# Kernel tuning notes

Hardware: AMD Instinct MI355X
Metric: run time of the kernel (lower is better)

Reference implementation:

```python
import jax, jax.numpy as jnp
import numpy as np

B, N, D = 8, 1024, 768      # batch, n_patches, prototype dim
V, C, Hh = 30000, 512, 768  # vocab size, clip_text_dim, proj hidden dim
TEMPERATURE = 0.2
BN_EPS = 1e-5


def _l2norm(x, axis=-1, eps=1e-12):
    # matches torch F.normalize (clamp_min on the norm)
    n = jnp.linalg.norm(x, axis=axis, keepdims=True)
    return x / jnp.maximum(n, eps)


def setup_inputs() -> dict:
    key = jax.random.key(0)
    k = jax.random.split(key, 6)
    patch_tokens = jax.random.normal(k[0], (B, N, D), dtype=jnp.float32)
    vocab_clip_embeddings = jax.random.normal(k[1], (V, C), dtype=jnp.float32)
    # ProjectionHead params: Linear(C->Hh, no bias) + BN(Hh) + ReLU + Linear(Hh->D, bias)
    W1 = jax.random.normal(k[2], (C, Hh), dtype=jnp.float32) / np.sqrt(C)
    bn_gamma = jnp.ones((Hh,), dtype=jnp.float32)
    bn_beta = jnp.zeros((Hh,), dtype=jnp.float32)
    W2 = jax.random.normal(k[3], (Hh, D), dtype=jnp.float32) / np.sqrt(Hh)
    b2 = jnp.zeros((D,), dtype=jnp.float32)
    return {
        "patch_tokens": patch_tokens,
        "vocab_clip_embeddings": vocab_clip_embeddings,
        "W1": W1,
        "bn_gamma": bn_gamma,
        "bn_beta": bn_beta,
        "W2": W2,
        "b2": b2,
    }


def reference(patch_tokens, vocab_clip_embeddings, W1, bn_gamma, bn_beta, W2, b2):
    # vocab CLIP embeddings are L2-normalized at module init
    vocab = _l2norm(vocab_clip_embeddings)            # [V, C]
    # ProjectionHead (training-mode BatchNorm over the V "batch" dim)
    h = vocab @ W1                                    # [V, Hh]
    mean = jnp.mean(h, axis=0)
    var = jnp.var(h, axis=0)                          # biased, as torch BN uses
    h = (h - mean) * (bn_gamma / jnp.sqrt(var + BN_EPS)) + bn_beta
    h = jax.nn.relu(h)
    prototypes = _l2norm(h @ W2 + b2)                 # [V, D]
    # normalize patch tokens, compute patch-prototype logits
    pt = _l2norm(patch_tokens)                        # [B, N, D]
    patch_prototype_logits = jnp.einsum("bnd,vd->bnv", pt, prototypes)  # [B, N, V]
    vocab_logits = jnp.max(patch_prototype_logits, axis=1)              # [B, V]
    mixture_weights = jax.nn.softmax(vocab_logits / TEMPERATURE, axis=-1)
    return mixture_weights
```

## Files before the change

kernel.cpp:

```cpp
#include <hip/hip_runtime.h>
#include <hip/hip_bf16.h>
#include <cstdint>


#define CDIV(a,b) (((a)+(b)-1)/(b))

using bf16x8 = __attribute__((ext_vector_type(8))) __bf16;
using f32x4  = __attribute__((ext_vector_type(4))) float;
using u16x8  = __attribute__((ext_vector_type(8))) unsigned short;
using u16x4  = __attribute__((ext_vector_type(4))) unsigned short;
using u32x4  = __attribute__((ext_vector_type(4))) unsigned;

__device__ __forceinline__ unsigned short f2bf(float x) {
  unsigned u = __float_as_uint(x);
  u += 0x7fffu + ((u >> 16) & 1u);
  return (unsigned short)(u >> 16);
}
__device__ __forceinline__ float bf2f(unsigned short b) {
  return __uint_as_float(((unsigned)b) << 16);
}
__device__ __forceinline__ unsigned fkey(float x) {
  unsigned u = __float_as_uint(x);
  return (u & 0x80000000u) ? ~u : (u | 0x80000000u);
}
__device__ __forceinline__ float fdec(unsigned k) {
  unsigned u = (k & 0x80000000u) ? (k ^ 0x80000000u) : ~k;
  return __uint_as_float(u);
}

__global__ __launch_bounds__(512, 1)
void gemm256_max_kernel(const unsigned short* __restrict__ A,
                        const unsigned short* __restrict__ B,
                        unsigned* __restrict__ maxkey)
{
  constexpr int K = 768, NT = 12, NXT = 118;
  __shared__ __align__(16) unsigned short lds[8 * 8192];

  const int tid = threadIdx.x;
  const int w = tid >> 6, lane = tid & 63;
  const int lr = lane & 15, kg = lane >> 4;
  const int wr = w >> 2, wc = w & 3;

  const int bid = blockIdx.x;
  const int wg = (bid & 7) * 472 + (bid >> 3);
  const long m0 = (long)(wg / NXT) * 256;
  const long n0 = (long)(wg % NXT) * 256;

  auto stage = [&](int slot, int tk, int mat, int h) {
    const unsigned short* src = mat ? B : A;
    const long row0 = mat ? n0 : m0;
    unsigned short* dst = lds + (((slot * 2) + mat) * 2 + h) * 8192;
#pragma unroll
    for (int ld = 0; ld < 2; ++ld) {
      const int lc  = ld * 512 + tid;
      const int row = lc >> 2;
      const int qc  = (lc & 3) ^ ((row >> 1) & 3);
      const unsigned short* gp = src + (row0 + row) * K + tk * 64 + h * 32 + qc * 8;
      __builtin_amdgcn_global_load_lds(
          (const __attribute__((address_space(1))) void*)gp,
          (__attribute__((address_space(3))) void*)(dst + (ld * 512 + (w << 6)) * 8),
          16, 0, 0);
    }
  };
  auto rdA = [&](int s, int h, int fm) -> bf16x8 {
    const int row = wr * 128 + fm * 16 + lr;
    const int pc  = kg ^ ((row >> 1) & 3);
    return *(const bf16x8*)(lds + ((s * 2 + 0) * 2 + h) * 8192 + row * 32 + pc * 8);
  };
  auto rdB = [&](int s, int h, int fn) -> bf16x8 {
    const int row = wc * 64 + fn * 16 + lr;
    const int pc  = kg ^ ((row >> 1) & 3);
    return *(const bf16x8*)(lds + ((s * 2 + 1) * 2 + h) * 8192 + row * 32 + pc * 8);
  };

  f32x4 acc[8][4];
#pragma unroll
  for (int i = 0; i < 8; ++i)
#pragma unroll
    for (int j = 0; j < 4; ++j) acc[i][j] = f32x4{0.f, 0.f, 0.f, 0.f};

  stage(0, 0, 0, 0); stage(0, 0, 1, 0); stage(0, 0, 0, 1);
  stage(0, 0, 1, 1); stage(1, 1, 0, 0); stage(1, 1, 1, 0);
  asm volatile("s_waitcnt vmcnt(8)" ::: "memory");
  __builtin_amdgcn_s_barrier();

  bf16x8 a[4], b[4];
  auto tile_body = [&](int t, int s) {
    const int t1c = (t + 1 < NT) ? t + 1 : NT - 1;
    const int t2c = (t + 2 < NT) ? t + 2 : NT - 1;
    const int s1  = s ^ 1;

#pragma unroll
    for (int i = 0; i < 4; ++i) a[i] = rdA(s, 0, i);
#pragma unroll
    for (int i = 0; i < 4; ++i) b[i] = rdB(s, 0, i);
    stage(s1, t1c, 0, 1);
    __builtin_amdgcn_s_barrier();
    asm volatile("s_waitcnt lgkmcnt(0)" ::: "memory");
    __builtin_amdgcn_sched_barrier(0);
    __builtin_amdgcn_s_setprio(1);
#pragma unroll
    for (int fm = 0; fm < 4; ++fm)
#pragma unroll
      for (int fn = 0; fn < 4; ++fn)
        acc[fm][fn] = __builtin_amdgcn_mfma_f32_16x16x32_bf16(a[fm], b[fn], acc[fm][fn], 0, 0, 0);
    __builtin_amdgcn_s_setprio(0);
    __builtin_amdgcn_sched_barrier(0);
    __builtin_amdgcn_s_barrier();

#pragma unroll
    for (int i = 0; i < 4; ++i) a[i] = rdA(s, 0, 4 + i);
    stage(s1, t1c, 1, 1);
    __builtin_amdgcn_s_barrier();
    asm volatile("s_waitcnt lgkmcnt(0)" ::: "memory");
    __builtin_amdgcn_sched_barrier(0);
    __builtin_amdgcn_s_setprio(1);
#pragma unroll
    for (int fm = 0; fm < 4; ++fm)
#pragma unroll
      for (int fn = 0; fn < 4; ++fn)
        acc[4 + fm][fn] = __builtin_amdgcn_mfma_f32_16x16x32_bf16(a[fm], b[fn], acc[4 + fm][fn], 0, 0, 0);
    __builtin_amdgcn_s_setprio(0);
    asm volatile("s_waitcnt vmcnt(8)" ::: "memory");
    __builtin_amdgcn_sched_barrier(0);
    __builtin_amdgcn_s_barrier();

#pragma unroll
    for (int i = 0; i < 4; ++i) a[i] = rdA(s, 1, i);
#pragma unroll
    for (int i = 0; i < 4; ++i) b[i] = rdB(s, 1, i);
    stage(s, t2c, 0, 0);
    __builtin_amdgcn_s_barrier();
    asm volatile("s_waitcnt lgkmcnt(0)" ::: "memory");
    __builtin_amdgcn_sched_barrier(0);
    __builtin_amdgcn_s_setprio(1);
#pragma unroll
    for (int fm = 0; fm < 4; ++fm)
#pragma unroll
      for (int fn = 0; fn < 4; ++fn)
        acc[fm][fn] = __builtin_amdgcn_mfma_f32_16x16x32_bf16(a[fm], b[fn], acc[fm][fn], 0, 0, 0);
    __builtin_amdgcn_s_setprio(0);
    __builtin_amdgcn_sched_barrier(0);
    __builtin_amdgcn_s_barrier();

#pragma unroll
    for (int i = 0; i < 4; ++i) a[i] = rdA(s, 1, 4 + i);
    stage(s, t2c, 1, 0);
    __builtin_amdgcn_s_barrier();
    asm volatile("s_waitcnt lgkmcnt(0)" ::: "memory");
    __builtin_amdgcn_sched_barrier(0);
    __builtin_amdgcn_s_setprio(1);
#pragma unroll
    for (int fm = 0; fm < 4; ++fm)
#pragma unroll
      for (int fn = 0; fn < 4; ++fn)
        acc[4 + fm][fn] = __builtin_amdgcn_mfma_f32_16x16x32_bf16(a[fm], b[fn], acc[4 + fm][fn], 0, 0, 0);
    __builtin_amdgcn_s_setprio(0);
    asm volatile("s_waitcnt vmcnt(8)" ::: "memory");
    __builtin_amdgcn_sched_barrier(0);
    __builtin_amdgcn_s_barrier();
  };

  for (int tt = 0; tt < NT; tt += 2) { tile_body(tt, 0); tile_body(tt + 1, 1); }

  const int bb = (int)(m0 >> 10);
#pragma unroll
  for (int fn = 0; fn < 4; ++fn) {
    float mx = acc[0][fn][0];
#pragma unroll
    for (int fm = 0; fm < 8; ++fm)
#pragma unroll
      for (int j = 0; j < 4; ++j) mx = fmaxf(mx, acc[fm][fn][j]);
    mx = fmaxf(mx, __shfl_xor(mx, 16));
    mx = fmaxf(mx, __shfl_xor(mx, 32));
    const long gn = n0 + wc * 64 + fn * 16 + lr;
    if (lane < 16)
      atomicMax(maxkey + (long)bb * 30208 + gn, fkey(mx));
  }
}

template<int EPI, bool STATS>
__global__ __launch_bounds__(256)
void gemm_nt_kernel(const unsigned short* __restrict__ A,
                    const unsigned short* __restrict__ B,
                    unsigned short* __restrict__ Cout,
                    const float* __restrict__ bias,
                    float* __restrict__ sums,
                    int M, int N, int K)
{
  __shared__ __align__(16) unsigned short As[128 * 32];
  __shared__ __align__(16) unsigned short Bs[128 * 32];
  const int tid  = threadIdx.x;
  const int w    = tid >> 6, lane = tid & 63;
  const int m0   = blockIdx.y * 128, n0 = blockIdx.x * 128;
  const int wr   = w >> 1, wc = w & 1;
  const int lrow = lane & 15, kg = lane >> 4;

  f32x4 acc[4][4];
#pragma unroll
  for (int i = 0; i < 4; ++i)
#pragma unroll
    for (int j = 0; j < 4; ++j) acc[i][j] = f32x4{0.f, 0.f, 0.f, 0.f};

  for (int k0 = 0; k0 < K; k0 += 32) {
#pragma unroll
    for (int i = 0; i < 2; ++i) {
      const int li = w * 2 + i;
      const int c  = li * 64 + lane;
      const int r  = c >> 2;
      const int kc = (c & 3) * 8;
      {
        int row = m0 + r; if (row > M - 1) row = M - 1;
        const unsigned short* gp = A + (size_t)row * K + (k0 + kc);
        __builtin_amdgcn_global_load_lds(
            (const __attribute__((address_space(1))) void*)gp,
            (__attribute__((address_space(3))) void*)(As + li * 512), 16, 0, 0);
      }
      {
        int row = n0 + r; if (row > N - 1) row = N - 1;
        const unsigned short* gp = B + (size_t)row * K + (k0 + kc);
        __builtin_amdgcn_global_load_lds(
            (const __attribute__((address_space(1))) void*)gp,
            (__attribute__((address_space(3))) void*)(Bs + li * 512), 16, 0, 0);
      }
    }
    __syncthreads();

    bf16x8 af[4], bfr[4];
#pragma unroll
    for (int fm = 0; fm < 4; ++fm)
      af[fm] = *(const bf16x8*)(As + (wr * 64 + fm * 16 + lrow) * 32 + kg * 8);
#pragma unroll
    for (int fn = 0; fn < 4; ++fn)
      bfr[fn] = *(const bf16x8*)(Bs + (wc * 64 + fn * 16 + lrow) * 32 + kg * 8);

#pragma unroll
    for (int fm = 0; fm < 4; ++fm)
#pragma unroll
      for (int fn = 0; fn < 4; ++fn)
        acc[fm][fn] = __builtin_amdgcn_mfma_f32_16x16x32_bf16(
            af[fm], bfr[fn], acc[fm][fn], 0, 0, 0);
    __syncthreads();
  }

#pragma unroll
  for (int fm = 0; fm < 4; ++fm) {
    const int gmb = m0 + wr * 64 + fm * 16 + kg * 4;
#pragma unroll
    for (int fn = 0; fn < 4; ++fn) {
      const int gn = n0 + wc * 64 + fn * 16 + lrow;
      const float bv = (EPI == 1) ? bias[gn] : 0.0f;
#pragma unroll
      for (int j = 0; j < 4; ++j) {
        const int gm = gmb + j;
        if (gm < M) Cout[(size_t)gm * N + gn] = f2bf(acc[fm][fn][j] + bv);
      }
    }
  }

  if (STATS) {
#pragma unroll
    for (int fn = 0; fn < 4; ++fn) {
      const int gn = n0 + wc * 64 + fn * 16 + lrow;
      float s = 0.f, q = 0.f;
#pragma unroll
      for (int fm = 0; fm < 4; ++fm) {
        const int gmb = m0 + wr * 64 + fm * 16 + kg * 4;
#pragma unroll
        for (int j = 0; j < 4; ++j) {
          if (gmb + j < M) {
            const float x = acc[fm][fn][j];
            s += x; q += x * x;
          }
        }
      }
      s += __shfl_xor(s, 16); s += __shfl_xor(s, 32);
      q += __shfl_xor(q, 16); q += __shfl_xor(q, 32);
      if (lane < 16 && gn < N) {
        atomicAdd(sums + gn, s);
        atomicAdd(sums + 768 + gn, q);
      }
    }
  }
}

template<int BLOCK, bool INBF>
__global__ __launch_bounds__(BLOCK)
void rownorm_kernel(const void* __restrict__ in, unsigned short* __restrict__ out,
                    int cols)
{
  __shared__ float red[BLOCK / 64];
  constexpr int VE = INBF ? 8 : 4;
  const int row = blockIdx.x, tid = threadIdx.x;
  const int nch = cols / VE;

  float x[VE];
  float ss = 0.f;
  if (tid < nch) {
    if (INBF) {
      const u16x8 v = ((const u16x8*)((const unsigned short*)in + (size_t)row * cols))[tid];
#pragma unroll
      for (int j = 0; j < 8; ++j) { x[j] = bf2f(v[j]); ss += x[j] * x[j]; }
    } else {
      const f32x4 v = ((const f32x4*)((const float*)in + (size_t)row * cols))[tid];
#pragma unroll
      for (int j = 0; j < 4; ++j) { x[j] = v[j]; ss += x[j] * x[j]; }
    }
  }
#pragma unroll
  for (int m = 32; m; m >>= 1) ss += __shfl_xor(ss, m);
  if ((tid & 63) == 0) red[tid >> 6] = ss;
  __syncthreads();
  float tot = 0.f;
#pragma unroll
  for (int i = 0; i < BLOCK / 64; ++i) tot += red[i];
  const float inv = 1.0f / fmaxf(sqrtf(tot), 1e-12f);

  if (tid < nch) {
    if (INBF) {
      u16x8 o;
#pragma unroll
      for (int j = 0; j < 8; ++j) o[j] = f2bf(x[j] * inv);
      ((u16x8*)(out + (size_t)row * cols))[tid] = o;
    } else {
      u16x4 o;
#pragma unroll
      for (int j = 0; j < 4; ++j) o[j] = f2bf(x[j] * inv);
      ((u16x4*)(out + (size_t)row * cols))[tid] = o;
    }
  }
}

__global__ __launch_bounds__(256)
void transpose_kernel(const float* __restrict__ in, unsigned short* __restrict__ out,
                      int R, int Cc)
{
  int i = blockIdx.x * 256 + threadIdx.x;
  if (i < R * Cc) {
    int r = i / Cc, c = i - r * Cc;
    out[(size_t)c * R + r] = f2bf(in[i]);
  }
}

__global__ __launch_bounds__(256)
void bnfinal_kernel(const float* __restrict__ sums, const float* __restrict__ gamma,
                    const float* __restrict__ beta, float* __restrict__ sc,
                    float* __restrict__ sh)
{
  const int ch = blockIdx.x * 256 + threadIdx.x;
  if (ch < 768) {
    const float invV = 1.0f / 30000.0f;
    const float mean = sums[ch] * invV;
    const float var  = sums[768 + ch] * invV - mean * mean;
    const float s    = gamma[ch] / sqrtf(var + 1e-5f);
    sc[ch] = s;
    sh[ch] = beta[ch] - mean * s;
  }
}

__global__ __launch_bounds__(256)
void bnapply_kernel(unsigned short* __restrict__ h, const float* __restrict__ sc,
                    const float* __restrict__ sh)
{
  const int total = 30000 * 96;
  for (int c = blockIdx.x * 256 + threadIdx.x; c < total; c += 2048 * 256) {
    const int ch = (c % 96) * 8;
    const u16x8 v = ((const u16x8*)h)[c];
    u16x8 o;
#pragma unroll
    for (int j = 0; j < 8; ++j) {
      const float y = fmaf(bf2f(v[j]), sc[ch + j], sh[ch + j]);
      o[j] = f2bf(fmaxf(y, 0.0f));
    }
    ((u16x8*)h)[c] = o;
  }
}

__global__ __launch_bounds__(256)
void smpart_kernel(const unsigned* __restrict__ mk, float* __restrict__ partsum)
{
  __shared__ float red[4];
  const int b = blockIdx.y;
  const unsigned* row = mk + (size_t)b * 30208 + blockIdx.x * 1000;
  float s = 0.f;
  for (int t = threadIdx.x; t < 1000; t += 256)
    s += expf((fdec(row[t]) - 1.0f) * 5.0f);
#pragma unroll
  for (int m = 32; m; m >>= 1) s += __shfl_xor(s, m);
  if ((threadIdx.x & 63) == 0) red[threadIdx.x >> 6] = s;
  __syncthreads();
  if (threadIdx.x == 0)
    atomicAdd(partsum + b, red[0] + red[1] + red[2] + red[3]);
}

__global__ __launch_bounds__(256)
void smfinal_kernel(const unsigned* __restrict__ mk, const float* __restrict__ partsum,
                    float* __restrict__ out)
{
  const int b = blockIdx.y;
  const int c = blockIdx.x * 256 + threadIdx.x;
  if (c < 3750) {
    const unsigned* row = mk + (size_t)b * 30208 + c * 8;
    const float inv = 1.0f / partsum[b];
    const u32x4 k0 = *(const u32x4*)row;
    const u32x4 k1 = *(const u32x4*)(row + 4);
    f32x4 o0, o1;
#pragma unroll
    for (int j = 0; j < 4; ++j) {
      o0[j] = expf((fdec(k0[j]) - 1.0f) * 5.0f) * inv;
      o1[j] = expf((fdec(k1[j]) - 1.0f) * 5.0f) * inv;
    }
    float* op = out + (size_t)b * 30000 + c * 8;
    *(f32x4*)op = o0;
    *(f32x4*)(op + 4) = o1;
  }
}

extern "C" void kernel_launch(void* const* d_in, const int* in_sizes, int n_in,
                              void* d_out, int out_size, void* d_ws, size_t ws_size,
                              hipStream_t stream)
{
  (void)in_sizes; (void)n_in; (void)out_size; (void)ws_size;
  const float* patch = (const float*)d_in[0];
  const float* vocab = (const float*)d_in[1];
  const float* W1    = (const float*)d_in[2];
  const float* gamma = (const float*)d_in[3];
  const float* beta  = (const float*)d_in[4];
  const float* W2    = (const float*)d_in[5];
  const float* b2    = (const float*)d_in[6];
  float* out = (float*)d_out;

  char* ws = (char*)d_ws;
  size_t off = 0;
  auto alloc = [&](size_t bytes) {
    char* p = ws + off;
    off += (bytes + 1023) & ~(size_t)1023;
    return p;
  };
  unsigned short* vocab_n = (unsigned short*)alloc(30000ull * 512 * 2);
  unsigned short* pt_n    = (unsigned short*)alloc(8192ull * 768 * 2);
  unsigned short* W1T     = (unsigned short*)alloc(768ull * 512 * 2);
  unsigned short* W2T     = (unsigned short*)alloc(768ull * 768 * 2);
  unsigned short* hbuf    = (unsigned short*)alloc(30000ull * 768 * 2);
  unsigned short* pbuf    = (unsigned short*)alloc(30000ull * 768 * 2);
  unsigned short* proto   = (unsigned short*)alloc(30208ull * 768 * 2);
  float*          bnsums  = (float*)alloc(768ull * 2 * 4);
  float*          bnsc    = (float*)alloc(768ull * 4);
  float*          bnsh    = (float*)alloc(768ull * 4);
  unsigned*       maxkey  = (unsigned*)alloc(8ull * 30208 * 4);
  float*          partsum = (float*)alloc(8ull * 4);

  hipMemsetAsync(bnsums, 0, 768ull * 2 * 4, stream);
  hipMemsetAsync(maxkey, 0, 8ull * 30208 * 4, stream);
  hipMemsetAsync(proto + 30000ull * 768, 0, 208ull * 768 * 2, stream);
  hipMemsetAsync(partsum, 0, 8ull * 4, stream);

  transpose_kernel<<<CDIV(512 * 768, 256), 256, 0, stream>>>(W1, W1T, 512, 768);
  transpose_kernel<<<CDIV(768 * 768, 256), 256, 0, stream>>>(W2, W2T, 768, 768);
  rownorm_kernel<256, false><<<30000, 256, 0, stream>>>(vocab, vocab_n, 512);
  rownorm_kernel<256, false><<<8192, 256, 0, stream>>>(patch, pt_n, 768);

  gemm_nt_kernel<0, true><<<dim3(6, 235), 256, 0, stream>>>(
      vocab_n, W1T, hbuf, nullptr, bnsums, 30000, 768, 512);
  bnfinal_kernel<<<3, 256, 0, stream>>>(bnsums, gamma, beta, bnsc, bnsh);
  bnapply_kernel<<<2048, 256, 0, stream>>>(hbuf, bnsc, bnsh);
  gemm_nt_kernel<1, false><<<dim3(6, 235), 256, 0, stream>>>(
      hbuf, W2T, pbuf, b2, nullptr, 30000, 768, 768);
  rownorm_kernel<128, true><<<30000, 128, 0, stream>>>(pbuf, proto, 768);

  gemm256_max_kernel<<<3776, 512, 0, stream>>>(pt_n, proto, maxkey);

  smpart_kernel<<<dim3(30, 8), 256, 0, stream>>>(maxkey, partsum);
  smfinal_kernel<<<dim3(15, 8), 256, 0, stream>>>(maxkey, partsum, out);
}
```

Baseline: 635.4 us.

## Reuse 256-tile pipelined GEMM for projection head and fold prototype norm into epilogue

The projection-head GEMMs now use the 256x256 pipelined MFMA kernel (templated by K, tile grid and epilogue) instead of the simple 128x128 kernel. The second GEMM's epilogue accumulates row sums of squares with atomics, so the separate prototype row-normalization pass is removed. The inverse norm is applied to the per-column max in the final GEMM epilogue; this is valid because the scale is positive. The two weight transposes are merged into one launch and the memsets into one, at the cost of a bf16 unnormalized prototype buffer and many extra atomics.

```diff
diff --git a/kernel.cpp b/kernel.cpp
--- a/kernel.cpp
+++ b/kernel.cpp
@@ -8,7 +8,6 @@
 using bf16x8 = __attribute__((ext_vector_type(8))) __bf16;
 using f32x4  = __attribute__((ext_vector_type(4))) float;
 using u16x8  = __attribute__((ext_vector_type(8))) unsigned short;
-using u16x4  = __attribute__((ext_vector_type(4))) unsigned short;
 using u32x4  = __attribute__((ext_vector_type(4))) unsigned;
 
 __device__ __forceinline__ unsigned short f2bf(float x) {
@@ -28,12 +27,17 @@
   return __uint_as_float(u);
 }
 
+template<int NT, int NXT, int EPI, int CPX>
 __global__ __launch_bounds__(512, 1)
-void gemm256_max_kernel(const unsigned short* __restrict__ A,
-                        const unsigned short* __restrict__ B,
-                        unsigned* __restrict__ maxkey)
-{
-  constexpr int K = 768, NT = 12, NXT = 118;
+void gemm8p_kernel(const unsigned short* __restrict__ A,
+                   const unsigned short* __restrict__ B,
+                   unsigned short* __restrict__ Cout,
+                   const float* __restrict__ bias,
+                   float* __restrict__ faux,
+                   unsigned* __restrict__ maxk,
+                   int aclamp)
+{
+  constexpr int K = NT * 64;
   __shared__ __align__(16) unsigned short lds[8 * 8192];
 
   const int tid = threadIdx.x;
@@ -42,7 +46,7 @@
   const int wr = w >> 2, wc = w & 3;
 
   const int bid = blockIdx.x;
-  const int wg = (bid & 7) * 472 + (bid >> 3);
+  const int wg = CPX ? ((bid & 7) * CPX + (bid >> 3)) : bid;
   const long m0 = (long)(wg / NXT) * 256;
   const long n0 = (long)(wg % NXT) * 256;
 
@@ -53,9 +57,10 @@
 #pragma unroll
     for (int ld = 0; ld < 2; ++ld) {
       const int lc  = ld * 512 + tid;
-      const int row = lc >> 2;
-      const int qc  = (lc & 3) ^ ((row >> 1) & 3);
-      const unsigned short* gp = src + (row0 + row) * K + tk * 64 + h * 32 + qc * 8;
+      long row = row0 + (lc >> 2);
+      if (!mat && row > aclamp) row = aclamp;
+      const int qc  = (lc & 3) ^ (((lc >> 2) >> 1) & 3);
+      const unsigned short* gp = src + row * K + tk * 64 + h * 32 + qc * 8;
       __builtin_amdgcn_global_load_lds(
           (const __attribute__((address_space(1))) void*)gp,
           (__attribute__((address_space(3))) void*)(dst + (ld * 512 + (w << 6)) * 8),
@@ -163,112 +168,43 @@
 
   for (int tt = 0; tt < NT; tt += 2) { tile_body(tt, 0); tile_body(tt + 1, 1); }
 
-  const int bb = (int)(m0 >> 10);
-#pragma unroll
-  for (int fn = 0; fn < 4; ++fn) {
-    float mx = acc[0][fn][0];
-#pragma unroll
-    for (int fm = 0; fm < 8; ++fm)
-#pragma unroll
-      for (int j = 0; j < 4; ++j) mx = fmaxf(mx, acc[fm][fn][j]);
-    mx = fmaxf(mx, __shfl_xor(mx, 16));
-    mx = fmaxf(mx, __shfl_xor(mx, 32));
-    const long gn = n0 + wc * 64 + fn * 16 + lr;
-    if (lane < 16)
-      atomicMax(maxkey + (long)bb * 30208 + gn, fkey(mx));
-  }
-}
-
-template<int EPI, bool STATS>
-__global__ __launch_bounds__(256)
-void gemm_nt_kernel(const unsigned short* __restrict__ A,
-                    const unsigned short* __restrict__ B,
-                    unsigned short* __restrict__ Cout,
-                    const float* __restrict__ bias,
-                    float* __restrict__ sums,
-                    int M, int N, int K)
-{
-  __shared__ __align__(16) unsigned short As[128 * 32];
-  __shared__ __align__(16) unsigned short Bs[128 * 32];
-  const int tid  = threadIdx.x;
-  const int w    = tid >> 6, lane = tid & 63;
-  const int m0   = blockIdx.y * 128, n0 = blockIdx.x * 128;
-  const int wr   = w >> 1, wc = w & 1;
-  const int lrow = lane & 15, kg = lane >> 4;
-
-  f32x4 acc[4][4];
-#pragma unroll
-  for (int i = 0; i < 4; ++i)
-#pragma unroll
-    for (int j = 0; j < 4; ++j) acc[i][j] = f32x4{0.f, 0.f, 0.f, 0.f};
-
-  for (int k0 = 0; k0 < K; k0 += 32) {
-#pragma unroll
-    for (int i = 0; i < 2; ++i) {
-      const int li = w * 2 + i;
-      const int c  = li * 64 + lane;
-      const int r  = c >> 2;
-      const int kc = (c & 3) * 8;
-      {
-        int row = m0 + r; if (row > M - 1) row = M - 1;
-        const unsigned short* gp = A + (size_t)row * K + (k0 + kc);
-        __builtin_amdgcn_global_load_lds(
-            (const __attribute__((address_space(1))) void*)gp,
-            (__attribute__((address_space(3))) void*)(As + li * 512), 16, 0, 0);
+  if (EPI == 2) {
+    const int bb = (int)(m0 >> 10);
+#pragma unroll
+    for (int fn = 0; fn < 4; ++fn) {
+      float mx = acc[0][fn][0];
+#pragma unroll
+      for (int fm = 0; fm < 8; ++fm)
+#pragma unroll
+        for (int j = 0; j < 4; ++j) mx = fmaxf(mx, acc[fm][fn][j]);
+      mx = fmaxf(mx, __shfl_xor(mx, 16));
+      mx = fmaxf(mx, __shfl_xor(mx, 32));
+      const long gn = n0 + wc * 64 + fn * 16 + lr;
+      if (lane < 16)
+        atomicMax(maxk + (long)bb * 30208 + gn, fkey(mx * faux[gn]));
+    }
+  } else if (EPI == 0) {
+#pragma unroll
+    for (int fm = 0; fm < 8; ++fm) {
+      const long gmb = m0 + wr * 128 + fm * 16 + kg * 4;
+#pragma unroll
+      for (int fn = 0; fn < 4; ++fn) {
+        const long gn = n0 + wc * 64 + fn * 16 + lr;
+#pragma unroll
+        for (int j = 0; j < 4; ++j)
+          Cout[(gmb + j) * (NXT * 256) + gn] = f2bf(acc[fm][fn][j]);
       }
-      {
-        int row = n0 + r; if (row > N - 1) row = N - 1;
-        const unsigned short* gp = B + (size_t)row * K + (k0 + kc);
-        __builtin_amdgcn_global_load_lds(
-            (const __attribute__((address_space(1))) void*)gp,
-            (__attribute__((address_space(3))) void*)(Bs + li * 512), 16, 0, 0);
-      }
-    }
-    __syncthreads();
-
-    bf16x8 af[4], bfr[4];
-#pragma unroll
-    for (int fm = 0; fm < 4; ++fm)
-      af[fm] = *(const bf16x8*)(As + (wr * 64 + fm * 16 + lrow) * 32 + kg * 8);
-#pragma unroll
-    for (int fn = 0; fn < 4; ++fn)
-      bfr[fn] = *(const bf16x8*)(Bs + (wc * 64 + fn * 16 + lrow) * 32 + kg * 8);
-
-#pragma unroll
-    for (int fm = 0; fm < 4; ++fm)
-#pragma unroll
-      for (int fn = 0; fn < 4; ++fn)
-        acc[fm][fn] = __builtin_amdgcn_mfma_f32_16x16x32_bf16(
-            af[fm], bfr[fn], acc[fm][fn], 0, 0, 0);
-    __syncthreads();
-  }
-
-#pragma unroll
-  for (int fm = 0; fm < 4; ++fm) {
-    const int gmb = m0 + wr * 64 + fm * 16 + kg * 4;
+    }
 #pragma unroll
     for (int fn = 0; fn < 4; ++fn) {
-      const int gn = n0 + wc * 64 + fn * 16 + lrow;
-      const float bv = (EPI == 1) ? bias[gn] : 0.0f;
-#pragma unroll
-      for (int j = 0; j < 4; ++j) {
-        const int gm = gmb + j;
-        if (gm < M) Cout[(size_t)gm * N + gn] = f2bf(acc[fm][fn][j] + bv);
-      }
-    }
-  }
-
-  if (STATS) {
-#pragma unroll
-    for (int fn = 0; fn < 4; ++fn) {
-      const int gn = n0 + wc * 64 + fn * 16 + lrow;
+      const long gn = n0 + wc * 64 + fn * 16 + lr;
       float s = 0.f, q = 0.f;
 #pragma unroll
-      for (int fm = 0; fm < 4; ++fm) {
-        const int gmb = m0 + wr * 64 + fm * 16 + kg * 4;
+      for (int fm = 0; fm < 8; ++fm) {
+        const long gmb = m0 + wr * 128 + fm * 16 + kg * 4;
 #pragma unroll
         for (int j = 0; j < 4; ++j) {
-          if (gmb + j < M) {
+          if (gmb + j <= aclamp) {
             const float x = acc[fm][fn][j];
             s += x; q += x * x;
           }
@@ -276,36 +212,52 @@
       }
       s += __shfl_xor(s, 16); s += __shfl_xor(s, 32);
       q += __shfl_xor(q, 16); q += __shfl_xor(q, 32);
-      if (lane < 16 && gn < N) {
-        atomicAdd(sums + gn, s);
-        atomicAdd(sums + 768 + gn, q);
+      if (lane < 16) {
+        atomicAdd(faux + gn, s);
+        atomicAdd(faux + 768 + gn, q);
       }
     }
-  }
-}
-
-template<int BLOCK, bool INBF>
+  } else {
+    float bv[4];
+#pragma unroll
+    for (int fn = 0; fn < 4; ++fn) bv[fn] = bias[n0 + wc * 64 + fn * 16 + lr];
+#pragma unroll
+    for (int fm = 0; fm < 8; ++fm) {
+      const long gmb = m0 + wr * 128 + fm * 16 + kg * 4;
+#pragma unroll
+      for (int j = 0; j < 4; ++j) {
+        const long gm = gmb + j;
+        float rs = 0.f;
+#pragma unroll
+        for (int fn = 0; fn < 4; ++fn) {
+          const long gn = n0 + wc * 64 + fn * 16 + lr;
+          const float x = acc[fm][fn][j] + bv[fn];
+          Cout[gm * (NXT * 256) + gn] = f2bf(x);
+          rs += x * x;
+        }
+        rs += __shfl_xor(rs, 1); rs += __shfl_xor(rs, 2);
+        rs += __shfl_xor(rs, 4); rs += __shfl_xor(rs, 8);
+        if (lr == 0) atomicAdd(faux + gm, rs);
+      }
+    }
+  }
+}
+
+template<int BLOCK>
 __global__ __launch_bounds__(BLOCK)
-void rownorm_kernel(const void* __restrict__ in, unsigned short* __restrict__ out,
+void rownorm_kernel(const float* __restrict__ in, unsigned short* __restrict__ out,
                     int cols)
 {
   __shared__ float red[BLOCK / 64];
-  constexpr int VE = INBF ? 8 : 4;
   const int row = blockIdx.x, tid = threadIdx.x;
-  const int nch = cols / VE;
-
-  float x[VE];
+  const int nch = cols / 4;
+
+  float x[4];
   float ss = 0.f;
   if (tid < nch) {
-    if (INBF) {
-      const u16x8 v = ((const u16x8*)((const unsigned short*)in + (size_t)row * cols))[tid];
-#pragma unroll
-      for (int j = 0; j < 8; ++j) { x[j] = bf2f(v[j]); ss += x[j] * x[j]; }
-    } else {
-      const f32x4 v = ((const f32x4*)((const float*)in + (size_t)row * cols))[tid];
-#pragma unroll
-      for (int j = 0; j < 4; ++j) { x[j] = v[j]; ss += x[j] * x[j]; }
-    }
+    const f32x4 v = ((const f32x4*)(in + (size_t)row * cols))[tid];
+#pragma unroll
+    for (int j = 0; j < 4; ++j) { x[j] = v[j]; ss += x[j] * x[j]; }
   }
 #pragma unroll
   for (int m = 32; m; m >>= 1) ss += __shfl_xor(ss, m);
@@ -317,28 +269,27 @@
   const float inv = 1.0f / fmaxf(sqrtf(tot), 1e-12f);
 
   if (tid < nch) {
-    if (INBF) {
-      u16x8 o;
-#pragma unroll
-      for (int j = 0; j < 8; ++j) o[j] = f2bf(x[j] * inv);
-      ((u16x8*)(out + (size_t)row * cols))[tid] = o;
-    } else {
-      u16x4 o;
-#pragma unroll
-      for (int j = 0; j < 4; ++j) o[j] = f2bf(x[j] * inv);
-      ((u16x4*)(out + (size_t)row * cols))[tid] = o;
-    }
-  }
-}
-
-__global__ __launch_bounds__(256)
-void transpose_kernel(const float* __restrict__ in, unsigned short* __restrict__ out,
-                      int R, int Cc)
-{
-  int i = blockIdx.x * 256 + threadIdx.x;
-  if (i < R * Cc) {
-    int r = i / Cc, c = i - r * Cc;
-    out[(size_t)c * R + r] = f2bf(in[i]);
+    __attribute__((ext_vector_type(4))) unsigned short o;
+#pragma unroll
+    for (int j = 0; j < 4; ++j) o[j] = f2bf(x[j] * inv);
+    ((decltype(o)*)(out + (size_t)row * cols))[tid] = o;
+  }
+}
+
+__global__ __launch_bounds__(256)
+void transpose2_kernel(const float* __restrict__ W1, const float* __restrict__ W2,
+                       unsigned short* __restrict__ W1T, unsigned short* __restrict__ W2T)
+{
+  const int i = blockIdx.x * 256 + threadIdx.x;
+  if (i < 512 * 768) {
+    const int r = i / 768, c = i - r * 768;
+    W1T[c * 512 + r] = f2bf(W1[i]);
+  } else {
+    const int k = i - 512 * 768;
+    if (k < 768 * 768) {
+      const int r = k / 768, c = k - r * 768;
+      W2T[c * 768 + r] = f2bf(W2[k]);
+    }
   }
 }
 
@@ -374,6 +325,13 @@
     }
     ((u16x8*)h)[c] = o;
   }
+}
+
+__global__ __launch_bounds__(256)
+void rfin_kernel(const float* __restrict__ rsum, float* __restrict__ rnorm)
+{
+  const int v = blockIdx.x * 256 + threadIdx.x;
+  if (v < 30208) rnorm[v] = 1.0f / fmaxf(sqrtf(rsum[v]), 1e-12f);
 }
 
 __global__ __launch_bounds__(256)
@@ -441,34 +399,34 @@
   unsigned short* pt_n    = (unsigned short*)alloc(8192ull * 768 * 2);
   unsigned short* W1T     = (unsigned short*)alloc(768ull * 512 * 2);
   unsigned short* W2T     = (unsigned short*)alloc(768ull * 768 * 2);
-  unsigned short* hbuf    = (unsigned short*)alloc(30000ull * 768 * 2);
-  unsigned short* pbuf    = (unsigned short*)alloc(30000ull * 768 * 2);
-  unsigned short* proto   = (unsigned short*)alloc(30208ull * 768 * 2);
-  float*          bnsums  = (float*)alloc(768ull * 2 * 4);
-  float*          bnsc    = (float*)alloc(768ull * 4);
-  float*          bnsh    = (float*)alloc(768ull * 4);
-  unsigned*       maxkey  = (unsigned*)alloc(8ull * 30208 * 4);
-  float*          partsum = (float*)alloc(8ull * 4);
-
-  hipMemsetAsync(bnsums, 0, 768ull * 2 * 4, stream);
-  hipMemsetAsync(maxkey, 0, 8ull * 30208 * 4, stream);
-  hipMemsetAsync(proto + 30000ull * 768, 0, 208ull * 768 * 2, stream);
-  hipMemsetAsync(partsum, 0, 8ull * 4, stream);
-
-  transpose_kernel<<<CDIV(512 * 768, 256), 256, 0, stream>>>(W1, W1T, 512, 768);
-  transpose_kernel<<<CDIV(768 * 768, 256), 256, 0, stream>>>(W2, W2T, 768, 768);
-  rownorm_kernel<256, false><<<30000, 256, 0, stream>>>(vocab, vocab_n, 512);
-  rownorm_kernel<256, false><<<8192, 256, 0, stream>>>(patch, pt_n, 768);
-
-  gemm_nt_kernel<0, true><<<dim3(6, 235), 256, 0, stream>>>(
-      vocab_n, W1T, hbuf, nullptr, bnsums, 30000, 768, 512);
+  unsigned short* hbuf    = (unsigned short*)alloc(30208ull * 768 * 2);
+  unsigned short* pbuf    = (unsigned short*)alloc(30208ull * 768 * 2);
+  float* zbase = (float*)alloc((1536ull + 30208 + 8 + 8ull * 30208) * 4);
+  float*    bnsums  = zbase;
+  float*    rsum    = zbase + 1536;
+  float*    partsum = zbase + 1536 + 30208;
+  unsigned* maxkey  = (unsigned*)(zbase + 1536 + 30208 + 8);
+  float*    bnsc    = (float*)alloc(768ull * 4);
+  float*    bnsh    = (float*)alloc(768ull * 4);
+  float*    rnorm   = (float*)alloc(30208ull * 4);
+
+  hipMemsetAsync(zbase, 0, (1536ull + 30208 + 8 + 8ull * 30208) * 4, stream);
+
+  transpose2_kernel<<<CDIV(512 * 768 + 768 * 768, 256), 256, 0, stream>>>(W1, W2, W1T, W2T);
+  rownorm_kernel<256><<<30000, 256, 0, stream>>>(vocab, vocab_n, 512);
+  rownorm_kernel<256><<<8192, 256, 0, stream>>>(patch, pt_n, 768);
+
+  gemm8p_kernel<8, 3, 0, 0><<<354, 512, 0, stream>>>(
+      vocab_n, W1T, hbuf, nullptr, bnsums, nullptr, 29999);
   bnfinal_kernel<<<3, 256, 0, stream>>>(bnsums, gamma, beta, bnsc, bnsh);
   bnapply_kernel<<<2048, 256, 0, stream>>>(hbuf, bnsc, bnsh);
-  gemm_nt_kernel<1, false><<<dim3(6, 235), 256, 0, stream>>>(
-      hbuf, W2T, pbuf, b2, nullptr, 30000, 768, 768);
-  rownorm_kernel<128, true><<<30000, 128, 0, stream>>>(pbuf, proto, 768);
-
-  gemm256_max_kernel<<<3776, 512, 0, stream>>>(pt_n, proto, maxkey);
+
+  gemm8p_kernel<12, 3, 1, 0><<<354, 512, 0, stream>>>(
+      hbuf, W2T, pbuf, b2, rsum, nullptr, 30207);
+  rfin_kernel<<<118, 256, 0, stream>>>(rsum, rnorm);
+
+  gemm8p_kernel<12, 118, 2, 472><<<3776, 512, 0, stream>>>(
+      pt_n, pbuf, nullptr, nullptr, rnorm, maxkey, 8191);
 
   smpart_kernel<<<dim3(30, 8), 256, 0, stream>>>(maxkey, partsum);
   smfinal_kernel<<<dim3(15, 8), 256, 0, stream>>>(maxkey, partsum, out);
```

New measurement: 592.1 us. 6.8% less time.
